# Optimization experiments

Hardware: AMD Instinct MI355X
Metric: run time of the kernel (lower is better)

Reference implementation:

```python
import jax, jax.numpy as jnp
import numpy as np


def setup_inputs() -> dict:
    key = jax.random.key(0)
    k1, k2 = jax.random.split(key)
    B, N, C = 128, 200000, 100
    values = jax.random.normal(k1, (B, N), dtype=jnp.float32)
    labels = jax.random.randint(k2, (N,), 0, C, dtype=jnp.int64)
    return {"values": values, "labels": labels, "num_classes": C}


def reference(values, labels, num_classes):
    # Stratified (label-grouped) max pooling:
    # values: [B, N], labels: [N] in [0, num_classes)
    # output: [B, num_classes], out[b, c] = max over columns j with labels[j] == c
    # segment_max reduces over the leading axis, so operate on values.T [N, B].
    pooled = jax.ops.segment_max(
        values.T, labels, num_segments=num_classes, indices_are_sorted=False
    )  # [C, B]
    return pooled.T  # [B, C]
```

## Files before the change

kernel.cpp:

```cpp
#include <hip/hip_runtime.h>
#include <hip/hip_bf16.h>


#define TPBS 256
#define COLS 256
#define ENC_NEG_INF 0x007FFFFFu

__device__ __forceinline__ unsigned enc(float f) {
    unsigned u = __float_as_uint(f);
    return (u & 0x80000000u) ? ~u : (u | 0x80000000u);
}
__device__ __forceinline__ float dec(unsigned u) {
    unsigned b = (u & 0x80000000u) ? (u & 0x7FFFFFFFu) : ~u;
    return __uint_as_float(b);
}

__global__ __launch_bounds__(TPBS) void strat_scat(
    const float* __restrict__ values, const int* __restrict__ labels,
    unsigned* __restrict__ part, int B, int N, int C, int S, int T) {
    extern __shared__ unsigned acc[];

    const int tid  = threadIdx.x;
    const int s    = blockIdx.x;
    const int rg   = blockIdx.y;
    const int row0 = rg * 64;
    const int rmax = min(64, B - row0);
    const int CW   = C * 65;

    for (int i = tid; i < CW; i += TPBS) acc[i] = ENC_NEG_INF;
    __syncthreads();

    for (int t = s; t < T; t += S) {
        const int jc = t * COLS + tid;
        if (jc < N) {
            const unsigned lab = (unsigned)labels[jc];
            unsigned* a = acc + lab * 65;
            const float* col = values + (size_t)row0 * N + jc;
            if (rmax == 64) {
#pragma unroll
                for (int rb = 0; rb < 64; rb += 16) {
                    float v[16];
#pragma unroll
                    for (int r = 0; r < 16; ++r)
                        v[r] = col[(size_t)(rb + r) * N];
#pragma unroll
                    for (int r = 0; r < 16; ++r)
                        atomicMax(&a[rb + r], enc(v[r]));
                }
            } else {
                for (int r = 0; r < rmax; ++r)
                    atomicMax(&a[r], enc(col[(size_t)r * N]));
            }
        }
    }
    __syncthreads();

    unsigned* dst = part + (size_t)(rg * S + s) * ((size_t)C * 64);
    for (int i = tid; i < C * 64; i += TPBS)
        dst[i] = acc[(i >> 6) * 65 + (i & 63)];
}

__global__ __launch_bounds__(256) void strat_red(
    const unsigned* __restrict__ part, float* __restrict__ out,
    int B, int C, int S, int RG) {
    const int PC = C * 64;
    const int i  = blockIdx.x * 256 + threadIdx.x;
    if (i >= RG * PC) return;
    const int rg  = i / PC;
    const int rem = i - rg * PC;
    const int c   = rem >> 6;
    const int l   = rem & 63;
    const int b   = rg * 64 + l;

    const unsigned* p = part + (size_t)rg * S * PC + rem;
    unsigned m0 = ENC_NEG_INF, m1 = ENC_NEG_INF, m2 = ENC_NEG_INF, m3 = ENC_NEG_INF;
    unsigned m4 = ENC_NEG_INF, m5 = ENC_NEG_INF, m6 = ENC_NEG_INF, m7 = ENC_NEG_INF;
    int s = 0;
    for (; s + 8 <= S; s += 8) {
        m0 = max(m0, p[(size_t)(s + 0) * PC]);
        m1 = max(m1, p[(size_t)(s + 1) * PC]);
        m2 = max(m2, p[(size_t)(s + 2) * PC]);
        m3 = max(m3, p[(size_t)(s + 3) * PC]);
        m4 = max(m4, p[(size_t)(s + 4) * PC]);
        m5 = max(m5, p[(size_t)(s + 5) * PC]);
        m6 = max(m6, p[(size_t)(s + 6) * PC]);
        m7 = max(m7, p[(size_t)(s + 7) * PC]);
    }
    for (; s < S; ++s) m0 = max(m0, p[(size_t)s * PC]);
    m0 = max(max(max(m0, m1), max(m2, m3)), max(max(m4, m5), max(m6, m7)));
    if (b < B) out[b * C + c] = dec(m0);
}


#define TPB   256
#define ROWS  8
#define FCPAD 257

__global__ __launch_bounds__(TPB) void strat_init(unsigned* __restrict__ out_enc, int n) {
    int i = blockIdx.x * TPB + threadIdx.x;
    if (i < n) out_enc[i] = ENC_NEG_INF;
}

__global__ __launch_bounds__(TPB) void strat_main_atomic(
    const float* __restrict__ values, const int* __restrict__ labels,
    unsigned* __restrict__ out_enc, int B, int N, int C, int T) {
    __shared__ unsigned acc[ROWS * FCPAD];
    const int tid  = threadIdx.x;
    const int row0 = blockIdx.y * ROWS;
    const int rmax = min(ROWS, B - row0);

    for (int i = tid; i < ROWS * FCPAD; i += TPB) acc[i] = ENC_NEG_INF;
    __syncthreads();

    const int t = blockIdx.x;
#pragma unroll
    for (int e = 0; e < 4; ++e) {
        const int j = t * 1024 + tid * 4 + e;
        if (j < N) {
            const int c = labels[j];
            for (int r = 0; r < rmax; ++r)
                atomicMax(&acc[r * FCPAD + c],
                          enc(values[(size_t)(row0 + r) * N + j]));
        }
    }
    __syncthreads();
    for (int i = tid; i < rmax * C; i += TPB) {
        const int r = i / C, c = i - r * C;
        atomicMax(&out_enc[(size_t)(row0 + r) * C + c], acc[r * FCPAD + c]);
    }
}

__global__ __launch_bounds__(TPB) void strat_decode(unsigned* __restrict__ buf, int n) {
    int i = blockIdx.x * TPB + threadIdx.x;
    if (i < n) {
        float f = dec(buf[i]);
        ((float*)buf)[i] = f;
    }
}


extern "C" void kernel_launch(void* const* d_in, const int* in_sizes, int n_in,
                              void* d_out, int out_size, void* d_ws, size_t ws_size,
                              hipStream_t stream) {
    const float* values = (const float*)d_in[0];
    const int*   labels = (const int*)d_in[1];
    const int N  = in_sizes[1];
    const int B  = in_sizes[0] / N;
    const int C  = out_size / B;
    const int T  = (N + COLS - 1) / COLS;
    const int RG = (B + 63) / 64;

    long total = (long)T * RG;
    int k = (int)((total + 1023) / 1024);
    if (k < 1) k = 1;
    int S = (T + k - 1) / k;
    size_t need = (size_t)RG * S * C * 64 * sizeof(unsigned);
    while (S > 1 && need > ws_size) {
        S = (S + 1) / 2;
        need = (size_t)RG * S * C * 64 * sizeof(unsigned);
    }

    const size_t lds = (size_t)C * 65 * sizeof(unsigned);
    const bool main_ok = (lds <= 64 * 1024) && (need <= ws_size) && (S >= 1);

    if (main_ok) {
        unsigned* part = (unsigned*)d_ws;
        dim3 grid(S, RG);
        strat_scat<<<grid, TPBS, lds, stream>>>(values, labels, part, B, N, C, S, T);
        const int outs = RG * C * 64;
        strat_red<<<(outs + 255) / 256, 256, 0, stream>>>(
            part, (float*)d_out, B, C, S, RG);
    } else {
        unsigned* out_enc = (unsigned*)d_out;
        const int init_blocks = (out_size + TPB - 1) / TPB;
        strat_init<<<init_blocks, TPB, 0, stream>>>(out_enc, out_size);
        dim3 grid((N + 1023) / 1024, (B + ROWS - 1) / ROWS);
        strat_main_atomic<<<grid, TPB, 0, stream>>>(values, labels, out_enc, B, N, C,
                                                    (N + 1023) / 1024);
        strat_decode<<<init_blocks, TPB, 0, stream>>>(out_enc, out_size);
    }
}
```

Measured before the change: 174.0 us.

## Split partial reduction into two stages and widen scatter blocks with prefetch

```diff
diff --git a/kernel.cpp b/kernel.cpp
--- a/kernel.cpp
+++ b/kernel.cpp
@@ -2,8 +2,9 @@
 #include <hip/hip_bf16.h>
 
 
-#define TPBS 256
-#define COLS 256
+#define TPBS 512
+#define COLS 512
+#define SB   16
 #define ENC_NEG_INF 0x007FFFFFu
 
 __device__ __forceinline__ unsigned enc(float f) {
@@ -17,11 +18,11 @@
 
 __global__ __launch_bounds__(TPBS) void strat_scat(
     const float* __restrict__ values, const int* __restrict__ labels,
-    unsigned* __restrict__ part, int B, int N, int C, int S, int T) {
+    unsigned* __restrict__ part, int B, int N, int C, int S) {
     extern __shared__ unsigned acc[];
 
     const int tid  = threadIdx.x;
-    const int s    = blockIdx.x;
+    const int t    = blockIdx.x;
     const int rg   = blockIdx.y;
     const int row0 = rg * 64;
     const int rmax = min(64, B - row0);
@@ -30,65 +31,83 @@
     for (int i = tid; i < CW; i += TPBS) acc[i] = ENC_NEG_INF;
     __syncthreads();
 
-    for (int t = s; t < T; t += S) {
-        const int jc = t * COLS + tid;
-        if (jc < N) {
-            const unsigned lab = (unsigned)labels[jc];
-            unsigned* a = acc + lab * 65;
-            const float* col = values + (size_t)row0 * N + jc;
-            if (rmax == 64) {
-#pragma unroll
-                for (int rb = 0; rb < 64; rb += 16) {
-                    float v[16];
+    const int jc = t * COLS + tid;
+    if (jc < N) {
+        const unsigned lab = (unsigned)labels[jc];
+        unsigned* a = acc + lab * 65;
+        const float* col = values + (size_t)row0 * N + jc;
+
+        if (rmax == 64) {
+            float v[2][16];
+#pragma unroll
+            for (int r = 0; r < 16; ++r) v[0][r] = col[(size_t)r * N];
+#pragma unroll
+            for (int b = 0; b < 4; ++b) {
+                const int cur = b & 1;
+                if (b < 3) {
 #pragma unroll
                     for (int r = 0; r < 16; ++r)
-                        v[r] = col[(size_t)(rb + r) * N];
-#pragma unroll
-                    for (int r = 0; r < 16; ++r)
-                        atomicMax(&a[rb + r], enc(v[r]));
+                        v[cur ^ 1][r] = col[(size_t)((b + 1) * 16 + r) * N];
                 }
-            } else {
-                for (int r = 0; r < rmax; ++r)
-                    atomicMax(&a[r], enc(col[(size_t)r * N]));
+#pragma unroll
+                for (int r = 0; r < 16; ++r)
+                    atomicMax(&a[b * 16 + r], enc(v[cur][r]));
             }
+        } else {
+            for (int r = 0; r < rmax; ++r)
+                atomicMax(&a[r], enc(col[(size_t)r * N]));
         }
     }
     __syncthreads();
 
-    unsigned* dst = part + (size_t)(rg * S + s) * ((size_t)C * 64);
+    unsigned* dst = part + (size_t)(rg * S + t) * ((size_t)C * 64);
     for (int i = tid; i < C * 64; i += TPBS)
         dst[i] = acc[(i >> 6) * 65 + (i & 63)];
 }
 
-__global__ __launch_bounds__(256) void strat_red(
-    const unsigned* __restrict__ part, float* __restrict__ out,
-    int B, int C, int S, int RG) {
-    const int PC = C * 64;
-    const int i  = blockIdx.x * 256 + threadIdx.x;
-    if (i >= RG * PC) return;
-    const int rg  = i / PC;
-    const int rem = i - rg * PC;
-    const int c   = rem >> 6;
-    const int l   = rem & 63;
-    const int b   = rg * 64 + l;
-
-    const unsigned* p = part + (size_t)rg * S * PC + rem;
+__global__ __launch_bounds__(256) void strat_redA(
+    const unsigned* __restrict__ part, unsigned* __restrict__ mid,
+    int PC, int S, int RG) {
+    const int total = RG * PC * SB;
+    const int i = blockIdx.x * 256 + threadIdx.x;
+    if (i >= total) return;
+    const int sb  = i / (RG * PC);
+    const int rem = i - sb * (RG * PC);
+    const int rg  = rem / PC;
+    const int q   = rem - rg * PC;
+
+    const int chunk = (S + SB - 1) / SB;
+    const int s0 = sb * chunk;
+    const int s1 = min(S, s0 + chunk);
+
+    const unsigned* p = part + ((size_t)rg * S) * PC + q;
     unsigned m0 = ENC_NEG_INF, m1 = ENC_NEG_INF, m2 = ENC_NEG_INF, m3 = ENC_NEG_INF;
-    unsigned m4 = ENC_NEG_INF, m5 = ENC_NEG_INF, m6 = ENC_NEG_INF, m7 = ENC_NEG_INF;
-    int s = 0;
-    for (; s + 8 <= S; s += 8) {
+    int s = s0;
+    for (; s + 4 <= s1; s += 4) {
         m0 = max(m0, p[(size_t)(s + 0) * PC]);
         m1 = max(m1, p[(size_t)(s + 1) * PC]);
         m2 = max(m2, p[(size_t)(s + 2) * PC]);
         m3 = max(m3, p[(size_t)(s + 3) * PC]);
-        m4 = max(m4, p[(size_t)(s + 4) * PC]);
-        m5 = max(m5, p[(size_t)(s + 5) * PC]);
-        m6 = max(m6, p[(size_t)(s + 6) * PC]);
-        m7 = max(m7, p[(size_t)(s + 7) * PC]);
-    }
-    for (; s < S; ++s) m0 = max(m0, p[(size_t)s * PC]);
-    m0 = max(max(max(m0, m1), max(m2, m3)), max(max(m4, m5), max(m6, m7)));
-    if (b < B) out[b * C + c] = dec(m0);
+    }
+    for (; s < s1; ++s) m0 = max(m0, p[(size_t)s * PC]);
+    mid[i] = max(max(m0, m1), max(m2, m3));
+}
+
+__global__ __launch_bounds__(256) void strat_redB(
+    const unsigned* __restrict__ mid, float* __restrict__ out,
+    int B, int C, int RG) {
+    const int PC = C * 64;
+    const int i = blockIdx.x * 256 + threadIdx.x;
+    if (i >= RG * PC) return;
+    unsigned m = ENC_NEG_INF;
+#pragma unroll
+    for (int sb = 0; sb < SB; ++sb) m = max(m, mid[(size_t)sb * RG * PC + i]);
+    const int rg = i / PC;
+    const int q  = i - rg * PC;
+    const int c  = q >> 6;
+    const int l  = q & 63;
+    const int b  = rg * 64 + l;
+    if (b < B) out[b * C + c] = dec(m);
 }
 
 
@@ -147,29 +166,29 @@
     const int N  = in_sizes[1];
     const int B  = in_sizes[0] / N;
     const int C  = out_size / B;
-    const int T  = (N + COLS - 1) / COLS;
     const int RG = (B + 63) / 64;
-
-    long total = (long)T * RG;
-    int k = (int)((total + 1023) / 1024);
-    if (k < 1) k = 1;
-    int S = (T + k - 1) / k;
-    size_t need = (size_t)RG * S * C * 64 * sizeof(unsigned);
-    while (S > 1 && need > ws_size) {
-        S = (S + 1) / 2;
-        need = (size_t)RG * S * C * 64 * sizeof(unsigned);
-    }
-
-    const size_t lds = (size_t)C * 65 * sizeof(unsigned);
-    const bool main_ok = (lds <= 64 * 1024) && (need <= ws_size) && (S >= 1);
+    const int PC = C * 64;
+    const int S  = (N + COLS - 1) / COLS;
+
+    const size_t part_bytes = (size_t)RG * S * PC * sizeof(unsigned);
+    const size_t mid_off    = (part_bytes + 255) & ~(size_t)255;
+    const size_t mid_bytes  = (size_t)SB * RG * PC * sizeof(unsigned);
+    const size_t lds        = (size_t)C * 65 * sizeof(unsigned);
+
+    const bool main_ok = (lds <= 64 * 1024) && (mid_off + mid_bytes <= ws_size);
 
     if (main_ok) {
         unsigned* part = (unsigned*)d_ws;
+        unsigned* mid  = (unsigned*)((char*)d_ws + mid_off);
+
         dim3 grid(S, RG);
-        strat_scat<<<grid, TPBS, lds, stream>>>(values, labels, part, B, N, C, S, T);
-        const int outs = RG * C * 64;
-        strat_red<<<(outs + 255) / 256, 256, 0, stream>>>(
-            part, (float*)d_out, B, C, S, RG);
+        strat_scat<<<grid, TPBS, lds, stream>>>(values, labels, part, B, N, C, S);
+
+        const int totalA = RG * PC * SB;
+        strat_redA<<<(totalA + 255) / 256, 256, 0, stream>>>(part, mid, PC, S, RG);
+
+        const int totalB = RG * PC;
+        strat_redB<<<(totalB + 255) / 256, 256, 0, stream>>>(mid, (float*)d_out, B, C, RG);
     } else {
         unsigned* out_enc = (unsigned*)d_out;
         const int init_blocks = (out_size + TPB - 1) / TPB;
```

New measurement: 165.6 us. -4.8%, faster.
